# Kernel tuning notes

Measured on AMD Instinct MI355X. Metric: run time of the kernel, lower is better.

## Reference

```python
import jax, jax.numpy as jnp
import numpy as np

BETA, ALPHA, NS_STEPS = 0.9, 1.0, 1
D_MODEL, D_STATE, D_CONV, EXPAND = 768, 16, 4, 2
D_INNER = EXPAND * D_MODEL
DT_RANK = -(-D_MODEL // 16)  # ceil(d_model/16) = 48
B, L = 2, 1024


def setup_inputs() -> dict:
    key = jax.random.key(0)
    ks = jax.random.split(key, 8)
    s = lambda k, shape, sc=0.02: jax.random.normal(k, shape, jnp.float32) * sc
    return {
        "hidden_states": jax.random.normal(ks[0], (B, L, D_MODEL), jnp.float32),
        "in_proj_w": s(ks[1], (2 * D_INNER, D_MODEL)),
        "conv_w": s(ks[2], (D_INNER, 1, D_CONV), 0.2),
        "conv_b": jnp.zeros((D_INNER,), jnp.float32),
        "x_proj_w": s(ks[3], (DT_RANK + 2 * D_STATE, D_INNER)),
        "dt_head_w": s(ks[4], (D_INNER, DT_RANK)),
        "dt_head_b": s(ks[5], (D_INNER,), 0.1),
        "out_proj_w": s(ks[6], (D_MODEL, D_INNER)),
        "D": jnp.ones((D_INNER,), jnp.float32),
    }


def _newton_schulz(G, steps):
    """Muon-style quintic Newton-Schulz orthogonalization of (b, d, n) with d >= n."""
    a, b, c = 3.4445, -4.7750, 2.0315
    X = G / (jnp.linalg.norm(G, axis=(-2, -1), keepdims=True) + 1e-7)
    X = X.swapaxes(-2, -1)  # (b, n, d): rows <= cols
    for _ in range(steps):
        A = X @ X.swapaxes(-2, -1)       # (b, n, n) small Gram
        Bm = b * A + c * (A @ A)
        X = a * X + Bm @ X
    return X.swapaxes(-2, -1)            # back to (b, d, n)


def reference(hidden_states, in_proj_w, conv_w, conv_b, x_proj_w, dt_head_w, dt_head_b, out_proj_w, D):
    Bz, Lz, _ = hidden_states.shape
    dtype = hidden_states.dtype
    # input projection -> x, z  (B, L, d_inner) each
    xz = jnp.einsum('bld,ed->ble', hidden_states, in_proj_w)
    x, z = jnp.split(xz, 2, axis=-1)
    # causal depthwise conv over time + SiLU
    xc = jax.lax.conv_general_dilated(
        x.swapaxes(1, 2), conv_w, (1,), [(D_CONV - 1, 0)],
        dimension_numbers=('NCH', 'OIH', 'NCH'), feature_group_count=D_INNER)
    x = jax.nn.silu(xc.swapaxes(1, 2) + conv_b)  # (B, L, d_inner)
    # projections for dt / k / q
    x_dbl = jnp.einsum('bld,ed->ble', x, x_proj_w)
    dt_low, k, q = jnp.split(x_dbl, [DT_RANK, DT_RANK + D_STATE], axis=-1)
    dt = jnp.einsum('blr,dr->bld', dt_low, dt_head_w)  # (B, L, d_inner), bias applied in scan

    def step(carry, inp):
        v, h = carry  # velocity / hidden states, each (b, d_inner, d_state)
        x_t, dt_t, k_t, q_t = inp
        dt_t = jax.nn.sigmoid(dt_t + dt_head_b)                              # (b, d)
        dt_t = dt_t / (1.0 + dt_t * jnp.sum(k_t * k_t, axis=-1, keepdims=True))
        dA = 1.0 - dt_t[:, :, None] * (k_t * k_t)[:, None, :]                # (b, d, n)
        G = (dt_t * x_t)[:, :, None] * k_t[:, None, :]                       # dt * u * k
        v = BETA * v + ALPHA * _newton_schulz(G, NS_STEPS)
        h = dA * h + v
        y_t = jnp.einsum('bdn,bn->bd', h, q_t) + D * x_t
        return (v, h), y_t

    init = (jnp.zeros((Bz, D_INNER, D_STATE), dtype),
            jnp.zeros((Bz, D_INNER, D_STATE), dtype))
    xs = (x.swapaxes(0, 1), dt.swapaxes(0, 1), k.swapaxes(0, 1), q.swapaxes(0, 1))
    _, y = jax.lax.scan(step, init, xs)        # (L, B, d_inner)
    y = y.swapaxes(0, 1) * jax.nn.silu(z)      # gate
    return jnp.einsum('bld,od->blo', y, out_proj_w)
```

## Files before the change

kernel.cpp:

```cpp
#include <hip/hip_runtime.h>

#define D_MODEL 768
#define D_STATE 16
#define D_INNER 1536
#define DT_RANK 48
#define NB 2
#define LSEQ 1024
#define NROWS (NB * LSEQ)
#define CCH 8
#define CLEN (LSEQ / CCH)
#define BETA_CL 1.3900845e-06f

typedef __attribute__((ext_vector_type(4))) float f32x4;
typedef __attribute__((ext_vector_type(8))) short s16x8;
typedef __attribute__((ext_vector_type(8))) unsigned short u16x8;

__device__ __forceinline__ unsigned short f2bu(float f) {
  unsigned int x = __builtin_bit_cast(unsigned int, f);
  x += 0x7fffu + ((x >> 16) & 1u);
  return (unsigned short)(x >> 16);
}
__device__ __forceinline__ float bfu(unsigned short u) {
  unsigned int x = ((unsigned int)u) << 16;
  return __builtin_bit_cast(float, x);
}

#define CVT_TOTAL 663552
#define Z1_GROUPS 20480
#define Z2_GROUPS 196608
__global__ __launch_bounds__(256) void cvt5z_kernel(const float* __restrict__ s0,
                                                    const float* __restrict__ s1,
                                                    const float* __restrict__ s2,
                                                    const float* __restrict__ s3,
                                                    const float* __restrict__ s4,
                                                    unsigned short* __restrict__ d0,
                                                    unsigned short* __restrict__ d1,
                                                    unsigned short* __restrict__ d2,
                                                    unsigned short* __restrict__ d3,
                                                    unsigned short* __restrict__ d4,
                                                    float* __restrict__ z1,
                                                    float* __restrict__ z2) {
  int g = blockIdx.x * 256 + threadIdx.x;
  if (g >= CVT_TOTAL) {
    int zg = g - CVT_TOTAL;
    f32x4 zero = {0.f, 0.f, 0.f, 0.f};
    if (zg < Z1_GROUPS) {
      *(f32x4*)(z1 + zg * 8) = zero;
      *(f32x4*)(z1 + zg * 8 + 4) = zero;
    } else if (zg < Z1_GROUPS + Z2_GROUPS) {
      int i = (zg - Z1_GROUPS) * 8;
      *(f32x4*)(z2 + i) = zero;
      *(f32x4*)(z2 + i + 4) = zero;
    }
    return;
  }
  const float* s;
  unsigned short* d;
  int base;
  if (g < 196608)      { s = s0; d = d0; base = 0; }
  else if (g < 491520) { s = s1; d = d1; base = 196608; }
  else if (g < 506880) { s = s2; d = d2; base = 491520; }
  else if (g < 516096) { s = s3; d = d3; base = 506880; }
  else                 { s = s4; d = d4; base = 516096; }
  int i = (g - base) * 8;
  f32x4 a = *(const f32x4*)(s + i);
  f32x4 b = *(const f32x4*)(s + i + 4);
  u16x8 o;
#pragma unroll
  for (int j = 0; j < 4; j++) { o[j] = f2bu(a[j]); o[4 + j] = f2bu(b[j]); }
  *(u16x8*)(d + i) = o;
}

template <bool ATOMIC>
__global__ __launch_bounds__(256) void gemm128(const unsigned short* __restrict__ A,
                                               const unsigned short* __restrict__ B,
                                               float* __restrict__ C, int K,
                                               int lda, int ldb, int ldc, int kseg_len) {
  __shared__ __align__(16) unsigned short As[2][128][40];
  __shared__ __align__(16) unsigned short Bs[2][128][40];
  const int m0 = blockIdx.y * 128, n0 = blockIdx.x * 128;
  const int kbeg = blockIdx.z * kseg_len;
  const int kend = kbeg + kseg_len;
  const int t = threadIdx.x;
  const int wave = t >> 6, lane = t & 63;
  const int wm = wave >> 1, wn = wave & 1;
  const int quad = lane >> 4, l16 = lane & 15;
  const int arow = t >> 1, kh = (t & 1) * 16;
  const unsigned short* Ap = A + (size_t)(m0 + arow) * lda + kh;
  const unsigned short* Bp = B + (size_t)(n0 + arow) * ldb + kh;

  u16x8 ra0, ra1, rb0, rb1;
  auto pref = [&](int k0) {
    ra0 = *(const u16x8*)(Ap + k0);
    ra1 = *(const u16x8*)(Ap + k0 + 8);
    rb0 = *(const u16x8*)(Bp + k0);
    rb1 = *(const u16x8*)(Bp + k0 + 8);
  };
  auto tolds = [&](int bi) {
    *(u16x8*)&As[bi][arow][kh] = ra0;
    *(u16x8*)&As[bi][arow][kh + 8] = ra1;
    *(u16x8*)&Bs[bi][arow][kh] = rb0;
    *(u16x8*)&Bs[bi][arow][kh + 8] = rb1;
  };

  f32x4 acc[4][4] = {};
  pref(kbeg);
  tolds(0);
  __syncthreads();
  int buf = 0;
  for (int k0 = kbeg; k0 < kend; k0 += 32) {
    const bool more = (k0 + 32 < kend);
    if (more) pref(k0 + 32);
    s16x8 af[4], bf[4];
#pragma unroll
    for (int i = 0; i < 4; i++) {
      af[i] = *(const s16x8*)&As[buf][wm * 64 + i * 16 + l16][quad * 8];
      bf[i] = *(const s16x8*)&Bs[buf][wn * 64 + i * 16 + l16][quad * 8];
    }
#pragma unroll
    for (int mi = 0; mi < 4; mi++)
#pragma unroll
      for (int ni = 0; ni < 4; ni++)
        acc[mi][ni] = __builtin_amdgcn_mfma_f32_16x16x32_bf16(af[mi], bf[ni], acc[mi][ni], 0, 0, 0);
    if (more) tolds(buf ^ 1);
    __syncthreads();
    buf ^= 1;
  }
#pragma unroll
  for (int mi = 0; mi < 4; mi++)
#pragma unroll
    for (int ni = 0; ni < 4; ni++)
#pragma unroll
      for (int r = 0; r < 4; r++) {
        int row = m0 + wm * 64 + mi * 16 + quad * 4 + r;
        int col = n0 + wn * 64 + ni * 16 + l16;
        if constexpr (ATOMIC)
          atomicAdd(&C[(size_t)row * ldc + col], acc[mi][ni][r]);
        else
          C[(size_t)row * ldc + col] = acc[mi][ni][r];
      }
}

template <bool ATOMIC>
__global__ __launch_bounds__(256) void gemm_bt(const unsigned short* __restrict__ Ab,
                                               const unsigned short* __restrict__ B,
                                               float* __restrict__ C, int M, int N, int K,
                                               int lda, int ldb, int ldc, int kseg_len) {
  __shared__ __align__(16) unsigned short As[2][64][40];
  __shared__ __align__(16) unsigned short Bs[2][64][40];
  const int m0 = blockIdx.y * 64, n0 = blockIdx.x * 64;
  const int kbeg = blockIdx.z * kseg_len;
  const int kend = (kbeg + kseg_len < K) ? (kbeg + kseg_len) : K;
  const int t = threadIdx.x;
  const int wave = t >> 6, lane = t & 63;
  const int wm = wave >> 1, wn = wave & 1;
  const int quad = lane >> 4, l16 = lane & 15;
  const int srow = t >> 2;
  const int kseg = (t & 3) * 8;
  const bool va = (m0 + srow) < M, vb = (n0 + srow) < N;
  const unsigned short* Bp = B + (size_t)(n0 + srow) * ldb;

  u16x8 rab, rbb;
  auto pref = [&](int k0) {
    const int kk = k0 + kseg;
    const int krem = kend - kk;
    const unsigned short* Ap = Ab + (size_t)(m0 + srow) * lda + kk;
    if (va && krem >= 8) {
      rab = *(const u16x8*)Ap;
    } else {
#pragma unroll
      for (int j = 0; j < 8; j++) rab[j] = (va && j < krem) ? Ap[j] : (unsigned short)0;
    }
    if (vb && krem >= 8) {
      rbb = *(const u16x8*)(Bp + kk);
    } else {
#pragma unroll
      for (int j = 0; j < 8; j++) rbb[j] = (vb && j < krem) ? Bp[kk + j] : (unsigned short)0;
    }
  };
  auto tolds = [&](int bi) {
    *(u16x8*)&As[bi][srow][kseg] = rab;
    *(u16x8*)&Bs[bi][srow][kseg] = rbb;
  };

  f32x4 acc[2][2] = {};
  pref(kbeg);
  tolds(0);
  __syncthreads();
  int buf = 0;
  for (int k0 = kbeg; k0 < kend; k0 += 32) {
    const bool more = (k0 + 32 < kend);
    if (more) pref(k0 + 32);
    s16x8 a0 = *(const s16x8*)&As[buf][wm * 32 + l16][quad * 8];
    s16x8 a1 = *(const s16x8*)&As[buf][wm * 32 + 16 + l16][quad * 8];
    s16x8 b0 = *(const s16x8*)&Bs[buf][wn * 32 + l16][quad * 8];
    s16x8 b1 = *(const s16x8*)&Bs[buf][wn * 32 + 16 + l16][quad * 8];
    acc[0][0] = __builtin_amdgcn_mfma_f32_16x16x32_bf16(a0, b0, acc[0][0], 0, 0, 0);
    acc[0][1] = __builtin_amdgcn_mfma_f32_16x16x32_bf16(a0, b1, acc[0][1], 0, 0, 0);
    acc[1][0] = __builtin_amdgcn_mfma_f32_16x16x32_bf16(a1, b0, acc[1][0], 0, 0, 0);
    acc[1][1] = __builtin_amdgcn_mfma_f32_16x16x32_bf16(a1, b1, acc[1][1], 0, 0, 0);
    if (more) tolds(buf ^ 1);
    __syncthreads();
    buf ^= 1;
  }
#pragma unroll
  for (int mi = 0; mi < 2; mi++)
#pragma unroll
    for (int ni = 0; ni < 2; ni++)
#pragma unroll
      for (int r = 0; r < 4; r++) {
        int row = m0 + wm * 32 + mi * 16 + quad * 4 + r;
        int col = n0 + wn * 32 + ni * 16 + l16;
        if (row < M && col < N) {
          if constexpr (ATOMIC)
            atomicAdd(&C[(size_t)row * ldc + col], acc[mi][ni][r]);
          else
            C[(size_t)row * ldc + col] = acc[mi][ni][r];
        }
      }
}

__global__ __launch_bounds__(256) void conv_silu_kernel(const float* __restrict__ xz,
                                                        const float* __restrict__ cw,
                                                        const float* __restrict__ cb,
                                                        float* __restrict__ xc,
                                                        unsigned short* __restrict__ xcb) {
  int idx = blockIdx.x * 256 + threadIdx.x;
  if (idx >= NROWS * D_INNER) return;
  int c = idx % D_INNER;
  int row = idx / D_INNER;
  int l = row & (LSEQ - 1);
  float acc = cb[c];
#pragma unroll
  for (int j = 0; j < 4; j++) {
    int dl = l - 3 + j;
    if (dl >= 0) acc += xz[(size_t)(row - 3 + j) * 3072 + c] * cw[c * 4 + j];
  }
  float sg = 1.0f / (1.0f + expf(-acc));
  float val = acc * sg;
  xc[idx] = val;
  xcb[idx] = f2bu(val);
}

__global__ __launch_bounds__(256) void precompute_kernel(const float* __restrict__ xdbl,
                                                         const unsigned short* __restrict__ wdt,
                                                         const float* __restrict__ xconv,
                                                         const float* __restrict__ dtb,
                                                         float* __restrict__ dtbuf,
                                                         float* __restrict__ ubuf,
                                                         float* __restrict__ kqbuf) {
  int row = blockIdx.x;
  int t = threadIdx.x;
  __shared__ float xr_s[80];
  if (t < 80) xr_s[t] = xdbl[(size_t)row * 80 + t];
  __syncthreads();
  float nk = 0.0f;
#pragma unroll
  for (int n = 0; n < 16; n++) { float kv = xr_s[48 + n]; nk += kv * kv; }
  float dtf[6], u0[6];
  float nupart = 0.0f;
#pragma unroll
  for (int i = 0; i < 6; i++) {
    int d = i * 256 + t;
    float draw = dtb[d];
    const unsigned short* w = wdt + (size_t)d * 48;
#pragma unroll
    for (int j = 0; j < 6; j++) {
      u16x8 wv = *(const u16x8*)(w + j * 8);
#pragma unroll
      for (int e = 0; e < 8; e++) draw = fmaf(bfu(wv[e]), xr_s[j * 8 + e], draw);
    }
    float sg = 1.0f / (1.0f + expf(-draw));
    float dv = sg / (1.0f + sg * nk);
    dtf[i] = dv;
    float u = dv * xconv[(size_t)row * D_INNER + d];
    u0[i] = u;
    nupart += u * u;
  }
  __shared__ float red[4];
  float v = nupart;
#pragma unroll
  for (int off = 32; off > 0; off >>= 1) v += __shfl_xor(v, off);
  if ((t & 63) == 0) red[t >> 6] = v;
  __syncthreads();
  float nu = red[0] + red[1] + red[2] + red[3];
  float p = nu * nk;
  float s = sqrtf(p) + 1e-7f;
  float tt = p / (s * s);
  float gamma = (3.4445f + tt * (-4.7750f + 2.0315f * tt)) / s;
#pragma unroll
  for (int i = 0; i < 6; i++) {
    int d = i * 256 + t;
    dtbuf[(size_t)row * D_INNER + d] = dtf[i];
    ubuf[(size_t)row * D_INNER + d] = gamma * u0[i];
  }
  if (t < 16) {
    kqbuf[(size_t)row * 32 + t] = xr_s[48 + t];
    kqbuf[(size_t)row * 32 + 16 + t] = xr_s[64 + t];
  }
}

__global__ __launch_bounds__(64) void scan_phase1(const float* __restrict__ ubuf,
                                                  const float* __restrict__ dtbuf,
                                                  const float* __restrict__ kqbuf,
                                                  float* __restrict__ cvp,
                                                  float* __restrict__ chp,
                                                  float* __restrict__ gp,
                                                  float* __restrict__ rp) {
  __shared__ float u_s[2][32][16];
  __shared__ float dt_s[2][32][16];
  __shared__ __align__(16) float kq_s[2][32][32];
  const int t = threadIdx.x;
  const int nq = t & 3, dloc = t >> 2;
  const int b = blockIdx.x / (96 * CCH);
  const int rem = blockIdx.x % (96 * CCH);
  const int d0 = (rem / CCH) * 16;
  const int c = rem % CCH;
  const int tbase = c * CLEN;
  const size_t ub = (size_t)b * LSEQ * D_INNER + d0;
  const float* kqb = kqbuf + (size_t)b * LSEQ * 32;
  const int scol = t & 15, srow0 = t >> 4;
  const int krow0 = t >> 3, kcol = (t & 7) * 4;
  float pu[8], pd[8];
  f32x4 pk[4];
  auto prefetch = [&](int t0) {
#pragma unroll
    for (int i = 0; i < 8; i++) {
      size_t off = ub + (size_t)(t0 + srow0 + 4 * i) * D_INNER + scol;
      pu[i] = ubuf[off];
      pd[i] = dtbuf[off];
    }
#pragma unroll
    for (int i = 0; i < 4; i++)
      pk[i] = *(const f32x4*)(kqb + (size_t)(t0 + krow0 + 8 * i) * 32 + kcol);
  };
  auto writelds = [&](int bi) {
#pragma unroll
    for (int i = 0; i < 8; i++) {
      u_s[bi][srow0 + 4 * i][scol] = pu[i];
      dt_s[bi][srow0 + 4 * i][scol] = pd[i];
    }
#pragma unroll
    for (int i = 0; i < 4; i++)
      *(f32x4*)&kq_s[bi][krow0 + 8 * i][kcol] = pk[i];
  };
  f32x4 v = {0.f, 0.f, 0.f, 0.f}, h = {0.f, 0.f, 0.f, 0.f};
  f32x4 g = {0.f, 0.f, 0.f, 0.f}, r = {1.f, 1.f, 1.f, 1.f};
  float bt = 0.9f;
  prefetch(tbase);
  writelds(0);
  int buf = 0;
  for (int t0 = 0; t0 < CLEN; t0 += 32) {
    const bool more = (t0 + 32 < CLEN);
    if (more) prefetch(tbase + t0 + 32);
#pragma unroll 4
    for (int s = 0; s < 32; s++) {
      float u = u_s[buf][s][dloc];
      float dtf = dt_s[buf][s][dloc];
      f32x4 kv = *(const f32x4*)&kq_s[buf][s][nq * 4];
#pragma unroll
      for (int j = 0; j < 4; j++) {
        float kj = kv[j];
        v[j] = fmaf(0.9f, v[j], u * kj);
        float a = fmaf(-dtf * kj, kj, 1.0f);
        h[j] = fmaf(a, h[j], v[j]);
        r[j] *= a;
        g[j] = fmaf(a, g[j], bt);
      }
      bt *= 0.9f;
    }
    if (more) writelds(buf ^ 1);
    buf ^= 1;
  }
  size_t o = (((size_t)b * CCH + c) * D_INNER + d0 + dloc) * 16 + nq * 4;
  *(f32x4*)(cvp + o) = v;
  *(f32x4*)(chp + o) = h;
  *(f32x4*)(gp + o) = g;
  *(f32x4*)(rp + o) = r;
}

__global__ __launch_bounds__(256) void scan_phase2(const float* __restrict__ cvp,
                                                   const float* __restrict__ chp,
                                                   float* __restrict__ gp,
                                                   float* __restrict__ rp) {
  int i = blockIdx.x * 256 + threadIdx.x;
  int b = i / (D_INNER * 16);
  int rem = i % (D_INNER * 16);
  float v0 = 0.f, h0 = 0.f;
#pragma unroll
  for (int c = 0; c < CCH; c++) {
    size_t o = ((size_t)(b * CCH + c)) * (D_INNER * 16) + rem;
    float cv = cvp[o], ch = chp[o], gg = gp[o], rr = rp[o];
    gp[o] = v0;
    rp[o] = h0;
    float v0n = fmaf(BETA_CL, v0, cv);
    float h0n = fmaf(gg, v0, fmaf(rr, h0, ch));
    v0 = v0n;
    h0 = h0n;
  }
}

__global__ __launch_bounds__(64) void scan_phase3(const float* __restrict__ ubuf,
                                                  const float* __restrict__ dtbuf,
                                                  const float* __restrict__ kqbuf,
                                                  const float* __restrict__ gp,
                                                  const float* __restrict__ rp,
                                                  const float* __restrict__ xconv,
                                                  const float* __restrict__ xz,
                                                  const float* __restrict__ Dp,
                                                  unsigned short* __restrict__ ygb) {
  __shared__ float u_s[2][32][16];
  __shared__ float dt_s[2][32][16];
  __shared__ float xc_s[2][32][16];
  __shared__ float z_s[2][32][16];
  __shared__ __align__(16) float kq_s[2][32][32];
  const int t = threadIdx.x;
  const int nq = t & 3, dloc = t >> 2;
  const int b = blockIdx.x / (96 * CCH);
  const int rem = blockIdx.x % (96 * CCH);
  const int d0 = (rem / CCH) * 16;
  const int c = rem % CCH;
  const int tbase = c * CLEN;
  const size_t ub = (size_t)b * LSEQ * D_INNER + d0;
  const float* kqb = kqbuf + (size_t)b * LSEQ * 32;
  unsigned short* y_p = ygb + (size_t)b * LSEQ * D_INNER + d0 + dloc;
  const float Dd = Dp[d0 + dloc];
  const int scol = t & 15, srow0 = t >> 4;
  const int krow0 = t >> 3, kcol = (t & 7) * 4;
  float pu[8], pd[8], pxc[8], pz[8];
  f32x4 pk[4];
  auto prefetch = [&](int t0) {
#pragma unroll
    for (int i = 0; i < 8; i++) {
      int lrow = t0 + srow0 + 4 * i;
      size_t off = ub + (size_t)lrow * D_INNER + scol;
      pu[i] = ubuf[off];
      pd[i] = dtbuf[off];
      pxc[i] = xconv[off];
      pz[i] = xz[((size_t)b * LSEQ + lrow) * 3072 + 1536 + d0 + scol];
    }
#pragma unroll
    for (int i = 0; i < 4; i++)
      pk[i] = *(const f32x4*)(kqb + (size_t)(t0 + krow0 + 8 * i) * 32 + kcol);
  };
  auto writelds = [&](int bi) {
#pragma unroll
    for (int i = 0; i < 8; i++) {
      u_s[bi][srow0 + 4 * i][scol] = pu[i];
      dt_s[bi][srow0 + 4 * i][scol] = pd[i];
      xc_s[bi][srow0 + 4 * i][scol] = pxc[i];
      z_s[bi][srow0 + 4 * i][scol] = pz[i];
    }
#pragma unroll
    for (int i = 0; i < 4; i++)
      *(f32x4*)&kq_s[bi][krow0 + 8 * i][kcol] = pk[i];
  };
  size_t so = (((size_t)b * CCH + c) * D_INNER + d0 + dloc) * 16 + nq * 4;
  f32x4 v = *(const f32x4*)(gp + so);
  f32x4 h = *(const f32x4*)(rp + so);
  prefetch(tbase);
  writelds(0);
  int buf = 0;
  for (int t0 = 0; t0 < CLEN; t0 += 32) {
    const bool more = (t0 + 32 < CLEN);
    if (more) prefetch(tbase + t0 + 32);
#pragma unroll 4
    for (int s = 0; s < 32; s++) {
      float u = u_s[buf][s][dloc];
      float dtf = dt_s[buf][s][dloc];
      f32x4 kv = *(const f32x4*)&kq_s[buf][s][nq * 4];
      f32x4 qv = *(const f32x4*)&kq_s[buf][s][16 + nq * 4];
      float yp = 0.0f;
#pragma unroll
      for (int j = 0; j < 4; j++) {
        float kj = kv[j];
        v[j] = fmaf(0.9f, v[j], u * kj);
        float dA = fmaf(-dtf * kj, kj, 1.0f);
        h[j] = fmaf(dA, h[j], v[j]);
        yp = fmaf(h[j], qv[j], yp);
      }
      yp += __shfl_xor(yp, 1);
      yp += __shfl_xor(yp, 2);
      if (nq == 0) {
        float z = z_s[buf][s][dloc];
        float sz = z / (1.0f + expf(-z));
        float val = (yp + Dd * xc_s[buf][s][dloc]) * sz;
        y_p[(size_t)(tbase + t0 + s) * D_INNER] = f2bu(val);
      }
    }
    if (more) writelds(buf ^ 1);
    buf ^= 1;
  }
}

extern "C" void kernel_launch(void* const* d_in, const int* in_sizes, int n_in,
                              void* d_out, int out_size, void* d_ws, size_t ws_size,
                              hipStream_t stream) {
  const float* hidden = (const float*)d_in[0];
  const float* w_in   = (const float*)d_in[1];
  const float* conv_w = (const float*)d_in[2];
  const float* conv_b = (const float*)d_in[3];
  const float* w_x    = (const float*)d_in[4];
  const float* w_dt   = (const float*)d_in[5];
  const float* b_dt   = (const float*)d_in[6];
  const float* w_out  = (const float*)d_in[7];
  const float* Dp     = (const float*)d_in[8];

  float* ws    = (float*)d_ws;
  float* xz    = ws;
  float* xconv = xz + (size_t)NROWS * 3072;
  float* xdbl  = xconv + (size_t)NROWS * D_INNER;
  float* dtbuf = xdbl + (size_t)NROWS * 80;
  float* ubuf  = dtbuf + (size_t)NROWS * D_INNER;
  float* kqbuf = ubuf + (size_t)NROWS * D_INNER;
  float* ybuf  = kqbuf + (size_t)NROWS * 32;
  const size_t PL = (size_t)NB * CCH * D_INNER * 16;
  float* cvp   = ybuf + (size_t)NROWS * D_INNER;
  float* chp   = cvp + PL;
  float* gp    = chp + PL;
  float* rp    = gp + PL;
  unsigned short* bfr = (unsigned short*)(rp + PL);
  unsigned short* hbf = bfr;
  unsigned short* wib = hbf + 1572864;
  unsigned short* wxb = wib + 2359296;
  unsigned short* wdb = wxb + 122880;
  unsigned short* wob = wdb + 73728;
  unsigned short* xcb = wob + 1179648;
  unsigned short* ygb = xcb + 3145728;

  dim3 blk(256);
  cvt5z_kernel<<<dim3((CVT_TOTAL + Z1_GROUPS + Z2_GROUPS) / 256), blk, 0, stream>>>(
      hidden, w_in, w_x, w_dt, w_out, hbf, wib, wxb, wdb, wob, xdbl, (float*)d_out);
  gemm128<false><<<dim3(24, 16, 1), blk, 0, stream>>>(hbf, wib, xz, 768, 768, 768, 3072, 768);
  conv_silu_kernel<<<dim3(12288), blk, 0, stream>>>(xz, conv_w, conv_b, xconv, xcb);
  gemm_bt<true><<<dim3(2, 32, 8), blk, 0, stream>>>(xcb, wxb, xdbl, 2048, 80, 1536,
                                                    1536, 1536, 80, 192);
  precompute_kernel<<<dim3(NROWS), blk, 0, stream>>>(xdbl, wdb, xconv, b_dt, dtbuf, ubuf, kqbuf);
  scan_phase1<<<dim3(NB * 96 * CCH), dim3(64), 0, stream>>>(ubuf, dtbuf, kqbuf, cvp, chp, gp, rp);
  scan_phase2<<<dim3(192), blk, 0, stream>>>(cvp, chp, gp, rp);
  scan_phase3<<<dim3(NB * 96 * CCH), dim3(64), 0, stream>>>(ubuf, dtbuf, kqbuf, gp, rp,
                                                            xconv, xz, Dp, ygb);
  gemm128<true><<<dim3(6, 16, 4), blk, 0, stream>>>(ygb, wob, (float*)d_out, 384,
                                                    1536, 1536, 768, 384);
}
```

Measured before the change: 246.8 us.

## Store scan inputs in channel-block-major layout and precompute gate terms in conv

The u and dt buffers now use a [batch][channel-block of 16][time][16] layout, so each scan block reads one contiguous stretch with vector loads instead of 16-float strided rows. The conv kernel also computes silu(z) and the D*x*silu(z) term in the same blocked layout, storing the latter as bf16. This removes the strided xz/xconv reads and the exp from the scan's phase 3. The cost is strided scattered writes in the conv and precompute kernels, plus lower precision on the skip term. gzblk reuses the hbf buffer, which is no longer needed once the first GEMM has run.

```diff
diff --git a/kernel.cpp b/kernel.cpp
--- a/kernel.cpp
+++ b/kernel.cpp
@@ -223,12 +223,16 @@
 __global__ __launch_bounds__(256) void conv_silu_kernel(const float* __restrict__ xz,
                                                         const float* __restrict__ cw,
                                                         const float* __restrict__ cb,
+                                                        const float* __restrict__ Dp,
                                                         float* __restrict__ xc,
-                                                        unsigned short* __restrict__ xcb) {
+                                                        unsigned short* __restrict__ xcb,
+                                                        float* __restrict__ szb,
+                                                        unsigned short* __restrict__ gzb) {
   int idx = blockIdx.x * 256 + threadIdx.x;
   if (idx >= NROWS * D_INNER) return;
   int c = idx % D_INNER;
   int row = idx / D_INNER;
+  int b = row >> 10;
   int l = row & (LSEQ - 1);
   float acc = cb[c];
 #pragma unroll
@@ -240,17 +244,24 @@
   float val = acc * sg;
   xc[idx] = val;
   xcb[idx] = f2bu(val);
+  float z = xz[(size_t)row * 3072 + 1536 + c];
+  float sz = z / (1.0f + expf(-z));
+  size_t bo = (((size_t)(b * 96 + (c >> 4))) * LSEQ + l) * 16 + (c & 15);
+  szb[bo] = sz;
+  gzb[bo] = f2bu(Dp[c] * val * sz);
 }
 
 __global__ __launch_bounds__(256) void precompute_kernel(const float* __restrict__ xdbl,
                                                          const unsigned short* __restrict__ wdt,
                                                          const float* __restrict__ xconv,
                                                          const float* __restrict__ dtb,
-                                                         float* __restrict__ dtbuf,
-                                                         float* __restrict__ ubuf,
+                                                         float* __restrict__ dtblk,
+                                                         float* __restrict__ ublk,
                                                          float* __restrict__ kqbuf) {
   int row = blockIdx.x;
   int t = threadIdx.x;
+  int b = row >> 10;
+  int l = row & (LSEQ - 1);
   __shared__ float xr_s[80];
   if (t < 80) xr_s[t] = xdbl[(size_t)row * 80 + t];
   __syncthreads();
@@ -291,8 +302,9 @@
 #pragma unroll
   for (int i = 0; i < 6; i++) {
     int d = i * 256 + t;
-    dtbuf[(size_t)row * D_INNER + d] = dtf[i];
-    ubuf[(size_t)row * D_INNER + d] = gamma * u0[i];
+    size_t bo = (((size_t)(b * 96 + (d >> 4))) * LSEQ + l) * 16 + (d & 15);
+    dtblk[bo] = dtf[i];
+    ublk[bo] = gamma * u0[i];
   }
   if (t < 16) {
     kqbuf[(size_t)row * 32 + t] = xr_s[48 + t];
@@ -300,46 +312,42 @@
   }
 }
 
-__global__ __launch_bounds__(64) void scan_phase1(const float* __restrict__ ubuf,
-                                                  const float* __restrict__ dtbuf,
+__global__ __launch_bounds__(64) void scan_phase1(const float* __restrict__ ublk,
+                                                  const float* __restrict__ dtblk,
                                                   const float* __restrict__ kqbuf,
                                                   float* __restrict__ cvp,
                                                   float* __restrict__ chp,
                                                   float* __restrict__ gp,
                                                   float* __restrict__ rp) {
-  __shared__ float u_s[2][32][16];
-  __shared__ float dt_s[2][32][16];
+  __shared__ float u_s[2][512];
+  __shared__ float dt_s[2][512];
   __shared__ __align__(16) float kq_s[2][32][32];
   const int t = threadIdx.x;
   const int nq = t & 3, dloc = t >> 2;
   const int b = blockIdx.x / (96 * CCH);
   const int rem = blockIdx.x % (96 * CCH);
-  const int d0 = (rem / CCH) * 16;
+  const int db = rem / CCH;
   const int c = rem % CCH;
   const int tbase = c * CLEN;
-  const size_t ub = (size_t)b * LSEQ * D_INNER + d0;
+  const float* ubp = ublk + (((size_t)(b * 96 + db)) * LSEQ + tbase) * 16;
+  const float* dtp = dtblk + (((size_t)(b * 96 + db)) * LSEQ + tbase) * 16;
   const float* kqb = kqbuf + (size_t)b * LSEQ * 32;
-  const int scol = t & 15, srow0 = t >> 4;
   const int krow0 = t >> 3, kcol = (t & 7) * 4;
-  float pu[8], pd[8];
-  f32x4 pk[4];
-  auto prefetch = [&](int t0) {
-#pragma unroll
-    for (int i = 0; i < 8; i++) {
-      size_t off = ub + (size_t)(t0 + srow0 + 4 * i) * D_INNER + scol;
-      pu[i] = ubuf[off];
-      pd[i] = dtbuf[off];
-    }
+  f32x4 pu0, pu1, pd0, pd1, pk[4];
+  auto prefetch = [&](int lt) {
+    pu0 = *(const f32x4*)(ubp + lt * 16 + t * 8);
+    pu1 = *(const f32x4*)(ubp + lt * 16 + t * 8 + 4);
+    pd0 = *(const f32x4*)(dtp + lt * 16 + t * 8);
+    pd1 = *(const f32x4*)(dtp + lt * 16 + t * 8 + 4);
 #pragma unroll
     for (int i = 0; i < 4; i++)
-      pk[i] = *(const f32x4*)(kqb + (size_t)(t0 + krow0 + 8 * i) * 32 + kcol);
+      pk[i] = *(const f32x4*)(kqb + (size_t)(tbase + lt + krow0 + 8 * i) * 32 + kcol);
   };
   auto writelds = [&](int bi) {
-#pragma unroll
-    for (int i = 0; i < 8; i++) {
-      u_s[bi][srow0 + 4 * i][scol] = pu[i];
-      dt_s[bi][srow0 + 4 * i][scol] = pd[i];
-    }
+    *(f32x4*)&u_s[bi][t * 8] = pu0;
+    *(f32x4*)&u_s[bi][t * 8 + 4] = pu1;
+    *(f32x4*)&dt_s[bi][t * 8] = pd0;
+    *(f32x4*)&dt_s[bi][t * 8 + 4] = pd1;
 #pragma unroll
     for (int i = 0; i < 4; i++)
       *(f32x4*)&kq_s[bi][krow0 + 8 * i][kcol] = pk[i];
@@ -347,16 +355,16 @@
   f32x4 v = {0.f, 0.f, 0.f, 0.f}, h = {0.f, 0.f, 0.f, 0.f};
   f32x4 g = {0.f, 0.f, 0.f, 0.f}, r = {1.f, 1.f, 1.f, 1.f};
   float bt = 0.9f;
-  prefetch(tbase);
+  prefetch(0);
   writelds(0);
   int buf = 0;
   for (int t0 = 0; t0 < CLEN; t0 += 32) {
     const bool more = (t0 + 32 < CLEN);
-    if (more) prefetch(tbase + t0 + 32);
+    if (more) prefetch(t0 + 32);
 #pragma unroll 4
     for (int s = 0; s < 32; s++) {
-      float u = u_s[buf][s][dloc];
-      float dtf = dt_s[buf][s][dloc];
+      float u = u_s[buf][s * 16 + dloc];
+      float dtf = dt_s[buf][s * 16 + dloc];
       f32x4 kv = *(const f32x4*)&kq_s[buf][s][nq * 4];
 #pragma unroll
       for (int j = 0; j < 4; j++) {
@@ -372,7 +380,7 @@
     if (more) writelds(buf ^ 1);
     buf ^= 1;
   }
-  size_t o = (((size_t)b * CCH + c) * D_INNER + d0 + dloc) * 16 + nq * 4;
+  size_t o = (((size_t)b * CCH + c) * D_INNER + db * 16 + dloc) * 16 + nq * 4;
   *(f32x4*)(cvp + o) = v;
   *(f32x4*)(chp + o) = h;
   *(f32x4*)(gp + o) = g;
@@ -400,74 +408,73 @@
   }
 }
 
-__global__ __launch_bounds__(64) void scan_phase3(const float* __restrict__ ubuf,
-                                                  const float* __restrict__ dtbuf,
+__global__ __launch_bounds__(64) void scan_phase3(const float* __restrict__ ublk,
+                                                  const float* __restrict__ dtblk,
                                                   const float* __restrict__ kqbuf,
                                                   const float* __restrict__ gp,
                                                   const float* __restrict__ rp,
-                                                  const float* __restrict__ xconv,
-                                                  const float* __restrict__ xz,
-                                                  const float* __restrict__ Dp,
+                                                  const float* __restrict__ szb,
+                                                  const unsigned short* __restrict__ gzb,
                                                   unsigned short* __restrict__ ygb) {
-  __shared__ float u_s[2][32][16];
-  __shared__ float dt_s[2][32][16];
-  __shared__ float xc_s[2][32][16];
-  __shared__ float z_s[2][32][16];
+  __shared__ float u_s[2][512];
+  __shared__ float dt_s[2][512];
+  __shared__ float sz_s[2][512];
+  __shared__ unsigned short gz_s[2][512];
   __shared__ __align__(16) float kq_s[2][32][32];
   const int t = threadIdx.x;
   const int nq = t & 3, dloc = t >> 2;
   const int b = blockIdx.x / (96 * CCH);
   const int rem = blockIdx.x % (96 * CCH);
-  const int d0 = (rem / CCH) * 16;
+  const int db = rem / CCH;
   const int c = rem % CCH;
   const int tbase = c * CLEN;
-  const size_t ub = (size_t)b * LSEQ * D_INNER + d0;
+  const size_t blkoff = (((size_t)(b * 96 + db)) * LSEQ + tbase) * 16;
+  const float* ubp = ublk + blkoff;
+  const float* dtp = dtblk + blkoff;
+  const float* szp = szb + blkoff;
+  const unsigned short* gzp = gzb + blkoff;
   const float* kqb = kqbuf + (size_t)b * LSEQ * 32;
-  unsigned short* y_p = ygb + (size_t)b * LSEQ * D_INNER + d0 + dloc;
-  const float Dd = Dp[d0 + dloc];
-  const int scol = t & 15, srow0 = t >> 4;
+  unsigned short* y_p = ygb + (size_t)b * LSEQ * D_INNER + db * 16 + dloc;
   const int krow0 = t >> 3, kcol = (t & 7) * 4;
-  float pu[8], pd[8], pxc[8], pz[8];
-  f32x4 pk[4];
-  auto prefetch = [&](int t0) {
-#pragma unroll
-    for (int i = 0; i < 8; i++) {
-      int lrow = t0 + srow0 + 4 * i;
-      size_t off = ub + (size_t)lrow * D_INNER + scol;
-      pu[i] = ubuf[off];
-      pd[i] = dtbuf[off];
-      pxc[i] = xconv[off];
-      pz[i] = xz[((size_t)b * LSEQ + lrow) * 3072 + 1536 + d0 + scol];
-    }
+  f32x4 pu0, pu1, pd0, pd1, ps0, ps1, pk[4];
+  u16x8 pg;
+  auto prefetch = [&](int lt) {
+    pu0 = *(const f32x4*)(ubp + lt * 16 + t * 8);
+    pu1 = *(const f32x4*)(ubp + lt * 16 + t * 8 + 4);
+    pd0 = *(const f32x4*)(dtp + lt * 16 + t * 8);
+    pd1 = *(const f32x4*)(dtp + lt * 16 + t * 8 + 4);
+    ps0 = *(const f32x4*)(szp + lt * 16 + t * 8);
+    ps1 = *(const f32x4*)(szp + lt * 16 + t * 8 + 4);
+    pg = *(const u16x8*)(gzp + lt * 16 + t * 8);
 #pragma unroll
     for (int i = 0; i < 4; i++)
-      pk[i] = *(const f32x4*)(kqb + (size_t)(t0 + krow0 + 8 * i) * 32 + kcol);
+      pk[i] = *(const f32x4*)(kqb + (size_t)(tbase + lt + krow0 + 8 * i) * 32 + kcol);
   };
   auto writelds = [&](int bi) {
-#pragma unroll
-    for (int i = 0; i < 8; i++) {
-      u_s[bi][srow0 + 4 * i][scol] = pu[i];
-      dt_s[bi][srow0 + 4 * i][scol] = pd[i];
-      xc_s[bi][srow0 + 4 * i][scol] = pxc[i];
-      z_s[bi][srow0 + 4 * i][scol] = pz[i];
-    }
+    *(f32x4*)&u_s[bi][t * 8] = pu0;
+    *(f32x4*)&u_s[bi][t * 8 + 4] = pu1;
+    *(f32x4*)&dt_s[bi][t * 8] = pd0;
+    *(f32x4*)&dt_s[bi][t * 8 + 4] = pd1;
+    *(f32x4*)&sz_s[bi][t * 8] = ps0;
+    *(f32x4*)&sz_s[bi][t * 8 + 4] = ps1;
+    *(u16x8*)&gz_s[bi][t * 8] = pg;
 #pragma unroll
     for (int i = 0; i < 4; i++)
       *(f32x4*)&kq_s[bi][krow0 + 8 * i][kcol] = pk[i];
   };
-  size_t so = (((size_t)b * CCH + c) * D_INNER + d0 + dloc) * 16 + nq * 4;
+  size_t so = (((size_t)b * CCH + c) * D_INNER + db * 16 + dloc) * 16 + nq * 4;
   f32x4 v = *(const f32x4*)(gp + so);
   f32x4 h = *(const f32x4*)(rp + so);
-  prefetch(tbase);
+  prefetch(0);
   writelds(0);
   int buf = 0;
   for (int t0 = 0; t0 < CLEN; t0 += 32) {
     const bool more = (t0 + 32 < CLEN);
-    if (more) prefetch(tbase + t0 + 32);
+    if (more) prefetch(t0 + 32);
 #pragma unroll 4
     for (int s = 0; s < 32; s++) {
-      float u = u_s[buf][s][dloc];
-      float dtf = dt_s[buf][s][dloc];
+      float u = u_s[buf][s * 16 + dloc];
+      float dtf = dt_s[buf][s * 16 + dloc];
       f32x4 kv = *(const f32x4*)&kq_s[buf][s][nq * 4];
       f32x4 qv = *(const f32x4*)&kq_s[buf][s][16 + nq * 4];
       float yp = 0.0f;
@@ -482,9 +489,7 @@
       yp += __shfl_xor(yp, 1);
       yp += __shfl_xor(yp, 2);
       if (nq == 0) {
-        float z = z_s[buf][s][dloc];
-        float sz = z / (1.0f + expf(-z));
-        float val = (yp + Dd * xc_s[buf][s][dloc]) * sz;
+        float val = fmaf(yp, sz_s[buf][s * 16 + dloc], bfu(gz_s[buf][s * 16 + dloc]));
         y_p[(size_t)(tbase + t0 + s) * D_INNER] = f2bu(val);
       }
     }
@@ -510,12 +515,12 @@
   float* xz    = ws;
   float* xconv = xz + (size_t)NROWS * 3072;
   float* xdbl  = xconv + (size_t)NROWS * D_INNER;
-  float* dtbuf = xdbl + (size_t)NROWS * 80;
-  float* ubuf  = dtbuf + (size_t)NROWS * D_INNER;
-  float* kqbuf = ubuf + (size_t)NROWS * D_INNER;
-  float* ybuf  = kqbuf + (size_t)NROWS * 32;
+  float* dtblk = xdbl + (size_t)NROWS * 80;
+  float* ublk  = dtblk + (size_t)NROWS * D_INNER;
+  float* kqbuf = ublk + (size_t)NROWS * D_INNER;
+  float* szblk = kqbuf + (size_t)NROWS * 32;
   const size_t PL = (size_t)NB * CCH * D_INNER * 16;
-  float* cvp   = ybuf + (size_t)NROWS * D_INNER;
+  float* cvp   = szblk + (size_t)NROWS * D_INNER;
   float* chp   = cvp + PL;
   float* gp    = chp + PL;
   float* rp    = gp + PL;
@@ -527,19 +532,21 @@
   unsigned short* wob = wdb + 73728;
   unsigned short* xcb = wob + 1179648;
   unsigned short* ygb = xcb + 3145728;
+  unsigned short* gzblk = hbf;
 
   dim3 blk(256);
   cvt5z_kernel<<<dim3((CVT_TOTAL + Z1_GROUPS + Z2_GROUPS) / 256), blk, 0, stream>>>(
       hidden, w_in, w_x, w_dt, w_out, hbf, wib, wxb, wdb, wob, xdbl, (float*)d_out);
   gemm128<false><<<dim3(24, 16, 1), blk, 0, stream>>>(hbf, wib, xz, 768, 768, 768, 3072, 768);
-  conv_silu_kernel<<<dim3(12288), blk, 0, stream>>>(xz, conv_w, conv_b, xconv, xcb);
+  conv_silu_kernel<<<dim3(12288), blk, 0, stream>>>(xz, conv_w, conv_b, Dp,
+                                                    xconv, xcb, szblk, gzblk);
   gemm_bt<true><<<dim3(2, 32, 8), blk, 0, stream>>>(xcb, wxb, xdbl, 2048, 80, 1536,
                                                     1536, 1536, 80, 192);
-  precompute_kernel<<<dim3(NROWS), blk, 0, stream>>>(xdbl, wdb, xconv, b_dt, dtbuf, ubuf, kqbuf);
-  scan_phase1<<<dim3(NB * 96 * CCH), dim3(64), 0, stream>>>(ubuf, dtbuf, kqbuf, cvp, chp, gp, rp);
+  precompute_kernel<<<dim3(NROWS), blk, 0, stream>>>(xdbl, wdb, xconv, b_dt, dtblk, ublk, kqbuf);
+  scan_phase1<<<dim3(NB * 96 * CCH), dim3(64), 0, stream>>>(ublk, dtblk, kqbuf, cvp, chp, gp, rp);
   scan_phase2<<<dim3(192), blk, 0, stream>>>(cvp, chp, gp, rp);
-  scan_phase3<<<dim3(NB * 96 * CCH), dim3(64), 0, stream>>>(ubuf, dtbuf, kqbuf, gp, rp,
-                                                            xconv, xz, Dp, ygb);
+  scan_phase3<<<dim3(NB * 96 * CCH), dim3(64), 0, stream>>>(ublk, dtblk, kqbuf, gp, rp,
+                                                            szblk, gzblk, ygb);
   gemm128<true><<<dim3(6, 16, 4), blk, 0, stream>>>(ygb, wob, (float*)d_out, 384,
                                                     1536, 1536, 768, 384);
 }
```

New measurement: 241.0 us. -2.3%, faster.
